# Kernel tuning notes

Hardware: AMD Instinct MI355X
Metric: run time of the kernel (lower is better)

## Reference

```python
import jax, jax.numpy as jnp
import numpy as np

N = 4096
INPUT_DIM = 256
HID = 64        # per-head dim == hidden_dim
HEADS = 4
OUT = 256
AIN = 2 * HID   # hidden + positional concat


def sinusoidal_pe(n, d):
    pos = jnp.arange(n, dtype=jnp.float32)[:, None]
    div = jnp.exp(jnp.arange(0, d, 2, dtype=jnp.float32) * (-np.log(10000.0) / d))
    pe = jnp.zeros((n, d), dtype=jnp.float32)
    pe = pe.at[:, 0::2].set(jnp.sin(pos * div))
    pe = pe.at[:, 1::2].set(jnp.cos(pos * div))
    return pe


def layer_norm(x, g, b, eps=1e-5):
    m = x.mean(-1, keepdims=True)
    v = ((x - m) ** 2).mean(-1, keepdims=True)
    return (x - m) / jnp.sqrt(v + eps) * g + b


def setup_inputs() -> dict:
    key = jax.random.key(0)
    ks = jax.random.split(key, 24)
    s = 0.02
    inp = {
        'Z': jax.random.normal(ks[0], (N, INPUT_DIM), jnp.float32),
        'Z_g': jax.random.normal(ks[1], (N, HID), jnp.float32),
        'Z_c': jax.random.normal(ks[2], (N, HID), jnp.float32),
        'adjacency_matrix': jax.random.randint(ks[3], (N, N), 0, 2).astype(jnp.float32),
        'Wq': s * jax.random.normal(ks[4], (AIN, HID * HEADS), jnp.float32),
        'bq': jnp.zeros((HID * HEADS,), jnp.float32),
        'Wk': s * jax.random.normal(ks[5], (AIN, HID * HEADS), jnp.float32),
        'bk': jnp.zeros((HID * HEADS,), jnp.float32),
        'Wv': s * jax.random.normal(ks[6], (AIN, HID * HEADS), jnp.float32),
        'bv': jnp.zeros((HID * HEADS,), jnp.float32),
        'Wo': s * jax.random.normal(ks[7], (HID * HEADS, OUT), jnp.float32),
        'bo': jnp.zeros((OUT,), jnp.float32),
        'Wr': s * jax.random.normal(ks[8], (INPUT_DIM, OUT), jnp.float32),
        'br': jnp.zeros((OUT,), jnp.float32),
        'ln1_g': jnp.ones((OUT,), jnp.float32),
        'ln1_b': jnp.zeros((OUT,), jnp.float32),
        'ln2_g': jnp.ones((OUT,), jnp.float32),
        'ln2_b': jnp.zeros((OUT,), jnp.float32),
        'f1_w': s * jax.random.normal(ks[9], (OUT, OUT * 4), jnp.float32),
        'f1_b': jnp.zeros((OUT * 4,), jnp.float32),
        'f2_w': s * jax.random.normal(ks[10], (OUT * 4, OUT * 2), jnp.float32),
        'f2_b': jnp.zeros((OUT * 2,), jnp.float32),
        'f3_w': s * jax.random.normal(ks[11], (OUT * 2, OUT), jnp.float32),
        'f3_b': jnp.zeros((OUT,), jnp.float32),
        'structure_weight': jnp.asarray(0.1, jnp.float32),
    }
    return inp


def reference(Z, Z_g, Z_c, adjacency_matrix, Wq, bq, Wk, bk, Wv, bv, Wo, bo,
              Wr, br, ln1_g, ln1_b, ln2_g, ln2_b, f1_w, f1_b, f2_w, f2_b,
              f3_w, f3_b, structure_weight):
    n = Z.shape[0]
    pos = sinusoidal_pe(n, HID)                       # [N, HID]
    Zg_p = jnp.concatenate([Z_g, pos], axis=-1)       # [N, 2*HID]
    Zc_p = jnp.concatenate([Z_c, pos], axis=-1)

    Q = (Zc_p @ Wq + bq).reshape(n, HEADS, HID).transpose(1, 0, 2)  # [H,N,D]
    K = (Zg_p @ Wk + bk).reshape(n, HEADS, HID).transpose(1, 0, 2)
    V = (Zg_p @ Wv + bv).reshape(n, HEADS, HID).transpose(1, 0, 2)

    scores = jnp.einsum('hnd,hmd->hnm', Q, K) / jnp.sqrt(jnp.asarray(HID, jnp.float32))
    structure_mask = (adjacency_matrix == 0).astype(jnp.float32) * -1e9  # [N,N]
    scores = scores + structure_weight * structure_mask[None, :, :]

    attn = jax.nn.softmax(scores, axis=-1)            # [H,N,N]
    attended = jnp.einsum('hnm,hmd->hnd', attn, V)    # [H,N,D]
    attended = attended.transpose(1, 0, 2).reshape(n, HEADS * HID)

    out = attended @ Wo + bo
    residual = Z @ Wr + br
    out = layer_norm(out + residual, ln1_g, ln1_b)

    h = jax.nn.gelu(out @ f1_w + f1_b, approximate=False)
    h = jax.nn.gelu(h @ f2_w + f2_b, approximate=False)
    ffn = h @ f3_w + f3_b
    out = layer_norm(out + ffn, ln2_g, ln2_b)
    return out, attn
```

## Files before the change

### kernel.cpp

```cpp
#include <hip/hip_runtime.h>
#include <cmath>

typedef __attribute__((ext_vector_type(8))) short bf16x8;
typedef __attribute__((ext_vector_type(4))) float f32x4;

#define MFMA16(A,B,C) __builtin_amdgcn_mfma_f32_16x16x32_bf16(A,B,C,0,0,0)

__device__ __forceinline__ ushort f2bf(float x){
  union { float f; unsigned u; } v; v.f = x;
  unsigned r = (v.u + 0x7fffu + ((v.u >> 16) & 1u)) >> 16;
  return (ushort)r;
}
__device__ __forceinline__ float bf2f(ushort h){
  union { unsigned u; float f; } v; v.u = ((unsigned)h) << 16;
  return v.f;
}


__global__ __launch_bounds__(256) void k_cvtZ(const float* Z, ushort* AZ){
  int r = blockIdx.x, c = threadIdx.x;
  AZ[(size_t)r*512 + 256 + c] = f2bf(Z[(size_t)r*256 + c]);
}

__global__ __launch_bounds__(256) void k_transpose(const float* in, ushort* out,
                                                   int K, int N, int RS, int CO){
  __shared__ float t[32][33];
  int kb = blockIdx.x*32, nb = blockIdx.y*32;
  int tx = threadIdx.x & 31, ty = threadIdx.x >> 5;
  for (int i = ty; i < 32; i += 8){
    int k = kb + i, n = nb + tx;
    t[i][tx] = (k < K && n < N) ? in[(size_t)k*N + n] : 0.f;
  }
  __syncthreads();
  for (int i = ty; i < 32; i += 8){
    int n = nb + i, k = kb + tx;
    if (n < N && k < K) out[(size_t)n*RS + CO + k] = f2bf(t[tx][i]);
  }
}

__global__ void k_biasor(const float* bo, const float* br, float* out){
  int j = threadIdx.x;
  out[j] = bo[j] + br[j];
}

__global__ __launch_bounds__(256) void k_qkv(
    const float* Zg, const float* Zc,
    const float* Wq, const float* bq, const float* Wk, const float* bk,
    const float* Wv, const float* bv,
    ushort* qb, ushort* kbuf, ushort* vb){
  __shared__ float zcp[16][128], zgp[16][128];
  int r0 = blockIdx.x * 16;
  int t = threadIdx.x;
  for (int i = t; i < 2048; i += 256){
    int row = i >> 7, c = i & 127;
    float vc, vg;
    if (c < 64){
      vc = Zc[(size_t)(r0+row)*64 + c];
      vg = Zg[(size_t)(r0+row)*64 + c];
    } else {
      int ii = (c - 64) >> 1;
      float div = __expf(-0.28782313662425572f * (float)ii);
      float arg = (float)(r0 + row) * div;
      float pe = ((c - 64) & 1) ? cosf(arg) : sinf(arg);
      vc = pe; vg = pe;
    }
    zcp[row][c] = vc; zgp[row][c] = vg;
  }
  __syncthreads();
  float aq[16], ak[16], av[16];
  #pragma unroll
  for (int r = 0; r < 16; r++){ aq[r]=0.f; ak[r]=0.f; av[r]=0.f; }
  int j = t;
  #pragma unroll 4
  for (int k = 0; k < 128; k++){
    float wq = Wq[(size_t)k*256 + j];
    float wk = Wk[(size_t)k*256 + j];
    float wv = Wv[(size_t)k*256 + j];
    #pragma unroll
    for (int r = 0; r < 16; r++){
      float xc = zcp[r][k], xg = zgp[r][k];
      aq[r] = fmaf(xc, wq, aq[r]);
      ak[r] = fmaf(xg, wk, ak[r]);
      av[r] = fmaf(xg, wv, av[r]);
    }
  }
  int h = j >> 6, d = j & 63;
  float bqv = bq[j], bkv = bk[j], bvv = bv[j];
  #pragma unroll
  for (int r = 0; r < 16; r++){
    size_t base = ((size_t)h*4096 + (r0 + r))*64 + d;
    qb[base]   = f2bf((aq[r] + bqv) * 0.125f);
    kbuf[base] = f2bf(ak[r] + bkv);
    vb[base]   = f2bf(av[r] + bvv);
  }
}

__global__ __launch_bounds__(256) void k_vtrans(const ushort* vb, ushort* vtb){
  __shared__ ushort t[64][65];
  int h = blockIdx.y, n0 = blockIdx.x * 64;
  int tx = threadIdx.x & 63, ty = threadIdx.x >> 6;
  for (int i = ty; i < 64; i += 4)
    t[i][tx] = vb[((size_t)h*4096 + n0 + i)*64 + tx];
  __syncthreads();
  for (int i = ty; i < 64; i += 4)
    vtb[((size_t)h*64 + i)*4096 + n0 + tx] = t[tx][i];
}

__global__ __launch_bounds__(1024, 4) void k_attn3(
    const ushort* qb, const ushort* kbuf, const ushort* vtb,
    const float* adj, float* attn_out, ushort* az){
  __shared__ __align__(16) char smem[16*4096*2];
  __shared__ float red[16][16];
  __shared__ float rsl[16];
  ushort* pbf = (ushort*)smem;
  float (*pvp)[16][66] = (float(*)[16][66])smem;

  int bid = blockIdx.x;
  int xcd = bid & 7, slot = bid >> 3;
  int nb = xcd*32 + (slot >> 2);
  int h  = slot & 3;
  int n0 = nb * 16;

  int t = threadIdx.x;
  int wave = t >> 6, lane = t & 63, lr = lane & 15, lg = lane >> 4;

  const ushort* Qh = qb   + ((size_t)h*4096 + n0)*64;
  const ushort* Kh = kbuf + (size_t)h*4096*64;
  const ushort* Vt = vtb  + (size_t)h*64*4096;
  float* aout = attn_out + (size_t)h*4096*4096 + (size_t)n0*4096;

  bf16x8 afr0 = *(const bf16x8*)(Qh + (size_t)lr*64 +  0 + lg*8);
  bf16x8 afr1 = *(const bf16x8*)(Qh + (size_t)lr*64 + 32 + lg*8);

  float rsum[4] = {0.f, 0.f, 0.f, 0.f};
  #pragma unroll 2
  for (int ct = 0; ct < 16; ct++){
    int cw = ct*256 + wave*16;
    const ushort* kp = Kh + (size_t)(cw + lr)*64 + lg*8;
    bf16x8 b0 = *(const bf16x8*)(kp);
    bf16x8 b1 = *(const bf16x8*)(kp + 32);
    const float* ap = adj + (size_t)(n0 + lg*4)*4096 + cw + lr;
    float a0 = ap[0], a1 = ap[4096], a2 = ap[8192], a3 = ap[12288];
    f32x4 acc = {0.f, 0.f, 0.f, 0.f};
    acc = MFMA16(afr0, b0, acc);
    acc = MFMA16(afr1, b1, acc);
    float p0 = a0 * __expf(acc[0]);
    float p1 = a1 * __expf(acc[1]);
    float p2 = a2 * __expf(acc[2]);
    float p3 = a3 * __expf(acc[3]);
    rsum[0] += p0; rsum[1] += p1; rsum[2] += p2; rsum[3] += p3;
    int col = cw + lr;
    float p4[4] = {p0, p1, p2, p3};
    #pragma unroll
    for (int r = 0; r < 4; r++){
      int row = lg*4 + r;
      pbf[row*4096 + (col ^ ((row & 7) << 3))] = f2bf(p4[r]);
    }
  }
  #pragma unroll
  for (int m = 1; m <= 8; m <<= 1){
    #pragma unroll
    for (int r = 0; r < 4; r++) rsum[r] += __shfl_xor(rsum[r], m, 64);
  }
  if (lr == 0){
    #pragma unroll
    for (int r = 0; r < 4; r++) red[wave][lg*4 + r] = rsum[r];
  }
  __syncthreads();
  if (t < 16){
    float s = 0.f;
    #pragma unroll
    for (int w2 = 0; w2 < 16; w2++) s += red[w2][t];
    rsl[t] = 1.f / s;
  }
  __syncthreads();

  {
    int row = wave;
    float iv = rsl[row];
    int swz = (row & 7) << 3;
    #pragma unroll 2
    for (int q = 0; q < 16; q++){
      int c = q*256 + lane*4;
      const ushort* src = &pbf[row*4096 + (c ^ swz)];
      ushort s4[4];
      *(uint2*)s4 = *(const uint2*)src;
      f32x4 ov = {bf2f(s4[0])*iv, bf2f(s4[1])*iv, bf2f(s4[2])*iv, bf2f(s4[3])*iv};
      __builtin_nontemporal_store(ov, (f32x4*)(aout + (size_t)row*4096 + c));
    }
  }

  f32x4 pacc[4];
  #pragma unroll
  for (int d = 0; d < 4; d++) pacc[d] = (f32x4){0.f,0.f,0.f,0.f};
  #pragma unroll
  for (int ks = 0; ks < 8; ks++){
    int kb2 = wave*256 + ks*32;
    bf16x8 pa = *(const bf16x8*)&pbf[lr*4096 + ((kb2 + lg*8) ^ ((lr & 7) << 3))];
    #pragma unroll
    for (int df = 0; df < 4; df++){
      bf16x8 v8 = *(const bf16x8*)(Vt + (size_t)(df*16 + lr)*4096 + kb2 + lg*8);
      pacc[df] = MFMA16(pa, v8, pacc[df]);
    }
  }

  __syncthreads();
  #pragma unroll
  for (int df = 0; df < 4; df++)
    #pragma unroll
    for (int r = 0; r < 4; r++)
      pvp[wave][lg*4 + r][df*16 + lr] = pacc[df][r];
  __syncthreads();
  {
    int row = t >> 6;
    int d   = t & 63;
    float s = 0.f;
    #pragma unroll
    for (int w2 = 0; w2 < 16; w2++) s += pvp[w2][row][d];
    s *= rsl[row];
    az[(size_t)(n0 + row)*512 + h*64 + d] = f2bf(s);
  }
}

__global__ __launch_bounds__(256) void k_gemm(
    const ushort* A, const ushort* Bt, const float* bias,
    const float* res, float* outf, ushort* outb,
    int M, int N, int K, int mode){
  __shared__ __align__(16) ushort la[64][40];
  __shared__ __align__(16) ushort lb[64][40];
  int mb = blockIdx.x * 64, nb = blockIdx.y * 64;
  int t = threadIdx.x;
  int wave = t >> 6, lane = t & 63, lr = lane & 15, lg = lane >> 4;
  int wm = (wave >> 1) * 32, wn = (wave & 1) * 32;
  f32x4 acc[2][2];
  #pragma unroll
  for (int i = 0; i < 2; i++)
    #pragma unroll
    for (int j = 0; j < 2; j++) acc[i][j] = (f32x4){0.f,0.f,0.f,0.f};

  int srow = t >> 2, scol = (t & 3) * 8;
  for (int k0 = 0; k0 < K; k0 += 32){
    *(bf16x8*)&la[srow][scol] = *(const bf16x8*)(A  + (size_t)(mb+srow)*K + k0 + scol);
    *(bf16x8*)&lb[srow][scol] = *(const bf16x8*)(Bt + (size_t)(nb+srow)*K + k0 + scol);
    __syncthreads();
    #pragma unroll
    for (int i = 0; i < 2; i++){
      bf16x8 af = *(const bf16x8*)&la[wm + i*16 + lr][lg*8];
      #pragma unroll
      for (int j = 0; j < 2; j++){
        bf16x8 bfg = *(const bf16x8*)&lb[wn + j*16 + lr][lg*8];
        acc[i][j] = MFMA16(af, bfg, acc[i][j]);
      }
    }
    __syncthreads();
  }

  #pragma unroll
  for (int i = 0; i < 2; i++)
    #pragma unroll
    for (int j = 0; j < 2; j++){
      int col = nb + wn + j*16 + lr;
      float bv = bias[col];
      #pragma unroll
      for (int r = 0; r < 4; r++){
        int row = mb + wm + i*16 + lg*4 + r;
        float v = acc[i][j][r] + bv;
        if (mode == 0){
          if (res) v += res[(size_t)row*N + col];
          outf[(size_t)row*N + col] = v;
        } else {
          float gl = 0.5f * v * (1.f + erff(v * 0.70710678118f));
          outb[(size_t)row*N + col] = f2bf(gl);
        }
      }
    }
}

__global__ __launch_bounds__(256) void k_ln(const float* X, const float* g, const float* b,
                                            float* outf, ushort* outb){
  int row = blockIdx.x * 4 + (threadIdx.x >> 6);
  int lane = threadIdx.x & 63;
  const float* xr = X + (size_t)row*256;
  f32x4 v = *(const f32x4*)(xr + lane*4);
  float s = v[0] + v[1] + v[2] + v[3];
  #pragma unroll
  for (int m = 32; m >= 1; m >>= 1) s += __shfl_xor(s, m, 64);
  float mean = s * (1.f/256.f);
  float d0[4]; float sq = 0.f;
  #pragma unroll
  for (int e = 0; e < 4; e++){ d0[e] = v[e] - mean; sq += d0[e]*d0[e]; }
  #pragma unroll
  for (int m = 32; m >= 1; m >>= 1) sq += __shfl_xor(sq, m, 64);
  float rstd = rsqrtf(sq * (1.f/256.f) + 1e-5f);
  float o[4];
  #pragma unroll
  for (int e = 0; e < 4; e++)
    o[e] = d0[e]*rstd*g[lane*4 + e] + b[lane*4 + e];
  if (outf){
    f32x4 ov = {o[0], o[1], o[2], o[3]};
    *(f32x4*)(outf + (size_t)row*256 + lane*4) = ov;
  }
  if (outb){
    union { ushort u[4]; uint2 q; } pk;
    #pragma unroll
    for (int e = 0; e < 4; e++) pk.u[e] = f2bf(o[e]);
    *(uint2*)(outb + (size_t)row*256 + lane*4) = pk.q;
  }
}

extern "C" void kernel_launch(void* const* d_in, const int* in_sizes, int n_in,
                              void* d_out, int out_size, void* d_ws, size_t ws_size,
                              hipStream_t stream){
  const float* Z    = (const float*)d_in[0];
  const float* Zg   = (const float*)d_in[1];
  const float* Zc   = (const float*)d_in[2];
  const float* adj  = (const float*)d_in[3];
  const float* Wq   = (const float*)d_in[4];
  const float* bq   = (const float*)d_in[5];
  const float* Wk   = (const float*)d_in[6];
  const float* bk   = (const float*)d_in[7];
  const float* Wv   = (const float*)d_in[8];
  const float* bv   = (const float*)d_in[9];
  const float* Wo   = (const float*)d_in[10];
  const float* bo   = (const float*)d_in[11];
  const float* Wr   = (const float*)d_in[12];
  const float* br   = (const float*)d_in[13];
  const float* ln1g = (const float*)d_in[14];
  const float* ln1b = (const float*)d_in[15];
  const float* ln2g = (const float*)d_in[16];
  const float* ln2b = (const float*)d_in[17];
  const float* f1w  = (const float*)d_in[18];
  const float* f1b  = (const float*)d_in[19];
  const float* f2w  = (const float*)d_in[20];
  const float* f2b  = (const float*)d_in[21];
  const float* f3w  = (const float*)d_in[22];
  const float* f3b  = (const float*)d_in[23];

  float* outF  = (float*)d_out;
  float* attnF = outF + (size_t)4096*256;

  const size_t MB = 1048576;
  char* w = (char*)d_ws;
  ushort* qb    = (ushort*)(w + 0*MB);
  ushort* kbuf  = (ushort*)(w + 2*MB);
  ushort* vtb   = (ushort*)(w + 4*MB);
  ushort* vb    = (ushort*)(w + 6*MB);
  ushort* h1    = (ushort*)(w + 0*MB);
  ushort* AZ    = (ushort*)(w + 8*MB);
  ushort* h2    = (ushort*)(w + 8*MB);
  ushort* BoR   = (ushort*)(w + 12*MB);
  float*  biasOR= (float*)(w + 12*MB + 262144);
  ushort* f1T   = (ushort*)(w + 13*MB);
  ushort* f2T   = (ushort*)(w + 13*MB + 524288);
  ushort* f3T   = (ushort*)(w + 14*MB + 524288);
  float*  X1    = (float*)(w + 15*MB);
  float*  yf    = (float*)(w + 19*MB);
  ushort* yb    = (ushort*)(w + 23*MB);

  k_cvtZ<<<4096, 256, 0, stream>>>(Z, AZ);
  k_transpose<<<dim3(8,  8), 256, 0, stream>>>(Wo,  BoR,  256,  256, 512,   0);
  k_transpose<<<dim3(8,  8), 256, 0, stream>>>(Wr,  BoR,  256,  256, 512, 256);
  k_transpose<<<dim3(8, 32), 256, 0, stream>>>(f1w, f1T,  256, 1024, 256,   0);
  k_transpose<<<dim3(32,16), 256, 0, stream>>>(f2w, f2T, 1024,  512, 1024,  0);
  k_transpose<<<dim3(16, 8), 256, 0, stream>>>(f3w, f3T,  512,  256, 512,   0);
  k_biasor<<<1, 256, 0, stream>>>(bo, br, biasOR);

  k_qkv<<<256, 256, 0, stream>>>(Zg, Zc, Wq, bq, Wk, bk, Wv, bv, qb, kbuf, vb);
  k_vtrans<<<dim3(64, 4), 256, 0, stream>>>(vb, vtb);

  k_attn3<<<1024, 1024, 0, stream>>>(qb, kbuf, vtb, adj, attnF, AZ);

  k_gemm<<<dim3(64, 4), 256, 0, stream>>>(AZ, BoR, biasOR, nullptr, X1, nullptr,
                                          4096, 256, 512, 0);
  k_ln<<<1024, 256, 0, stream>>>(X1, ln1g, ln1b, yf, yb);

  k_gemm<<<dim3(64,16), 256, 0, stream>>>(yb, f1T, f1b, nullptr, nullptr, h1,
                                          4096, 1024, 256, 1);
  k_gemm<<<dim3(64, 8), 256, 0, stream>>>(h1, f2T, f2b, nullptr, nullptr, h2,
                                          4096, 512, 1024, 1);
  k_gemm<<<dim3(64, 4), 256, 0, stream>>>(h2, f3T, f3b, yf, X1, nullptr,
                                          4096, 256, 512, 0);
  k_ln<<<1024, 256, 0, stream>>>(X1, ln2g, ln2b, outF, nullptr);
}
```

Baseline: 284.0 us.

## Fuse output-projection and FFN3 GEMMs with their LayerNorms into one kernel

Replaces the two GEMM+LayerNorm pairs with a single kernel that computes a 32-row by 256-column tile and applies bias, residual and LayerNorm in the epilogue, reducing the row statistics across waves through shared memory. This removes the fp32 intermediate round trip through global memory and two kernel launches. The trade-off is only 128 blocks with unpipelined, single-buffered K loads. Variance is now computed as E[x²]−mean², which is slightly less numerically stable.

Result: slower. 302.5 us (+6.5%).

```diff
diff --git a/kernel.cpp b/kernel.cpp
--- a/kernel.cpp
+++ b/kernel.cpp
@@ -276,36 +276,89 @@
     }
 }
 
-__global__ __launch_bounds__(256) void k_ln(const float* X, const float* g, const float* b,
-                                            float* outf, ushort* outb){
-  int row = blockIdx.x * 4 + (threadIdx.x >> 6);
-  int lane = threadIdx.x & 63;
-  const float* xr = X + (size_t)row*256;
-  f32x4 v = *(const f32x4*)(xr + lane*4);
-  float s = v[0] + v[1] + v[2] + v[3];
-  #pragma unroll
-  for (int m = 32; m >= 1; m >>= 1) s += __shfl_xor(s, m, 64);
-  float mean = s * (1.f/256.f);
-  float d0[4]; float sq = 0.f;
-  #pragma unroll
-  for (int e = 0; e < 4; e++){ d0[e] = v[e] - mean; sq += d0[e]*d0[e]; }
-  #pragma unroll
-  for (int m = 32; m >= 1; m >>= 1) sq += __shfl_xor(sq, m, 64);
-  float rstd = rsqrtf(sq * (1.f/256.f) + 1e-5f);
-  float o[4];
-  #pragma unroll
-  for (int e = 0; e < 4; e++)
-    o[e] = d0[e]*rstd*g[lane*4 + e] + b[lane*4 + e];
-  if (outf){
-    f32x4 ov = {o[0], o[1], o[2], o[3]};
-    *(f32x4*)(outf + (size_t)row*256 + lane*4) = ov;
-  }
-  if (outb){
-    union { ushort u[4]; uint2 q; } pk;
-    #pragma unroll
-    for (int e = 0; e < 4; e++) pk.u[e] = f2bf(o[e]);
-    *(uint2*)(outb + (size_t)row*256 + lane*4) = pk.q;
-  }
+__global__ __launch_bounds__(256) void k_gemm_ln(
+    const ushort* A, const ushort* Bt, const float* bias, const float* res,
+    const float* g, const float* b, float* outf, ushort* outb, int K){
+  __shared__ __align__(16) ushort la[32][40];
+  __shared__ __align__(16) ushort lb[256][40];
+  __shared__ float rsm[32][5];
+  __shared__ float rsq[32][5];
+  int mb = blockIdx.x * 32;
+  int t = threadIdx.x;
+  int wave = t >> 6, lane = t & 63, lr = lane & 15, lg = lane >> 4;
+
+  f32x4 acc[2][4];
+  #pragma unroll
+  for (int i = 0; i < 2; i++)
+    #pragma unroll
+    for (int j = 0; j < 4; j++) acc[i][j] = (f32x4){0.f,0.f,0.f,0.f};
+
+  int sr = t >> 2, sc = (t & 3) * 8;
+  for (int k0 = 0; k0 < K; k0 += 32){
+    if (t < 128)
+      *(bf16x8*)&la[sr][sc] = *(const bf16x8*)(A + (size_t)(mb+sr)*K + k0 + sc);
+    #pragma unroll
+    for (int q = 0; q < 4; q++)
+      *(bf16x8*)&lb[sr + 64*q][sc] = *(const bf16x8*)(Bt + (size_t)(sr+64*q)*K + k0 + sc);
+    __syncthreads();
+    #pragma unroll
+    for (int i = 0; i < 2; i++){
+      bf16x8 af = *(const bf16x8*)&la[i*16 + lr][lg*8];
+      #pragma unroll
+      for (int j = 0; j < 4; j++){
+        bf16x8 bfg = *(const bf16x8*)&lb[wave*64 + j*16 + lr][lg*8];
+        acc[i][j] = MFMA16(af, bfg, acc[i][j]);
+      }
+    }
+    __syncthreads();
+  }
+
+  float v[2][4][4];
+  #pragma unroll
+  for (int i = 0; i < 2; i++)
+    #pragma unroll
+    for (int r = 0; r < 4; r++){
+      int row = mb + i*16 + lg*4 + r;
+      float s = 0.f, q = 0.f;
+      #pragma unroll
+      for (int j = 0; j < 4; j++){
+        int col = wave*64 + j*16 + lr;
+        float x = acc[i][j][r] + bias[col];
+        if (res) x += res[(size_t)row*256 + col];
+        v[i][j][r] = x;
+        s += x; q += x*x;
+      }
+      #pragma unroll
+      for (int m = 1; m <= 8; m <<= 1){
+        s += __shfl_xor(s, m, 64);
+        q += __shfl_xor(q, m, 64);
+      }
+      if (lr == 0){
+        rsm[i*16 + lg*4 + r][wave] = s;
+        rsq[i*16 + lg*4 + r][wave] = q;
+      }
+    }
+  __syncthreads();
+
+  #pragma unroll
+  for (int i = 0; i < 2; i++)
+    #pragma unroll
+    for (int r = 0; r < 4; r++){
+      int rl = i*16 + lg*4 + r;
+      float tot  = rsm[rl][0] + rsm[rl][1] + rsm[rl][2] + rsm[rl][3];
+      float totq = rsq[rl][0] + rsq[rl][1] + rsq[rl][2] + rsq[rl][3];
+      float mean = tot * (1.f/256.f);
+      float var  = totq * (1.f/256.f) - mean*mean;
+      float rstd = rsqrtf(var + 1e-5f);
+      int row = mb + rl;
+      #pragma unroll
+      for (int j = 0; j < 4; j++){
+        int col = wave*64 + j*16 + lr;
+        float o = (v[i][j][r] - mean)*rstd*g[col] + b[col];
+        if (outf) outf[(size_t)row*256 + col] = o;
+        if (outb) outb[(size_t)row*256 + col] = f2bf(o);
+      }
+    }
 }
 
 extern "C" void kernel_launch(void* const* d_in, const int* in_sizes, int n_in,
@@ -353,9 +406,8 @@
   ushort* f1T   = (ushort*)(w + 13*MB);
   ushort* f2T   = (ushort*)(w + 13*MB + 524288);
   ushort* f3T   = (ushort*)(w + 14*MB + 524288);
-  float*  X1    = (float*)(w + 15*MB);
-  float*  yf    = (float*)(w + 19*MB);
-  ushort* yb    = (ushort*)(w + 23*MB);
+  float*  yf    = (float*)(w + 15*MB);
+  ushort* yb    = (ushort*)(w + 19*MB);
 
   k_cvtZ<<<4096, 256, 0, stream>>>(Z, AZ);
   k_transpose<<<dim3(8,  8), 256, 0, stream>>>(Wo,  BoR,  256,  256, 512,   0);
@@ -370,15 +422,13 @@
 
   k_attn3<<<1024, 1024, 0, stream>>>(qb, kbuf, vtb, adj, attnF, AZ);
 
-  k_gemm<<<dim3(64, 4), 256, 0, stream>>>(AZ, BoR, biasOR, nullptr, X1, nullptr,
-                                          4096, 256, 512, 0);
-  k_ln<<<1024, 256, 0, stream>>>(X1, ln1g, ln1b, yf, yb);
+  k_gemm_ln<<<128, 256, 0, stream>>>(AZ, BoR, biasOR, nullptr,
+                                     ln1g, ln1b, yf, yb, 512);
 
   k_gemm<<<dim3(64,16), 256, 0, stream>>>(yb, f1T, f1b, nullptr, nullptr, h1,
                                           4096, 1024, 256, 1);
   k_gemm<<<dim3(64, 8), 256, 0, stream>>>(h1, f2T, f2b, nullptr, nullptr, h2,
                                           4096, 512, 1024, 1);
-  k_gemm<<<dim3(64, 4), 256, 0, stream>>>(h2, f3T, f3b, yf, X1, nullptr,
-                                          4096, 256, 512, 0);
-  k_ln<<<1024, 256, 0, stream>>>(X1, ln2g, ln2b, outF, nullptr);
-}
+  k_gemm_ln<<<128, 256, 0, stream>>>(h2, f3T, f3b, yf,
+                                     ln2g, ln2b, outF, nullptr, 512);
+}
```
